# Optimization experiments

Hardware: AMD Instinct MI355X
Metric: run time of the kernel (lower is better)

The kernel has to match this reference:

```python
import jax, jax.numpy as jnp
import numpy as np

B, T, V, E, H, L = 128, 128, 5000, 256, 512, 128
PAD_IDX = 0


def setup_inputs() -> dict:
    key = jax.random.key(0)
    ks = jax.random.split(key, 12)
    s = 0.02  # init scale
    noise = jax.random.normal(ks[0], (B, L), dtype=jnp.float32)
    # Precomputed gumbel noise, one draw per (step, batch, vocab)
    u = jax.random.uniform(ks[1], (T, B, V), dtype=jnp.float32, minval=1e-9, maxval=1.0)
    gumbel = -jnp.log(-jnp.log(u))
    emb = (jax.random.normal(ks[2], (V, E), dtype=jnp.float32) * s).at[PAD_IDX].set(0.0)
    return {
        "noise": noise,
        "gumbel": gumbel,
        "temperature": jnp.float32(1.0),
        "W_init": jax.random.normal(ks[3], (H, L), dtype=jnp.float32) * s,
        "b_init": jnp.zeros((H,), dtype=jnp.float32),
        "emb": emb,
        "W_ih": jax.random.normal(ks[4], (3 * H, E), dtype=jnp.float32) * s,
        "W_hh": jax.random.normal(ks[5], (3 * H, H), dtype=jnp.float32) * s,
        "b_ih": jax.random.normal(ks[6], (3 * H,), dtype=jnp.float32) * s,
        "b_hh": jax.random.normal(ks[7], (3 * H,), dtype=jnp.float32) * s,
        "W_out": jax.random.normal(ks[8], (V, H), dtype=jnp.float32) * s,
        "b_out": jnp.zeros((V,), dtype=jnp.float32),
    }


def reference(noise, gumbel, temperature, W_init, b_init, emb, W_ih, W_hh, b_ih, b_hh, W_out, b_out):
    # h_0 = fc_initial_state(noise)  -> [B, H]
    h0 = noise @ W_init.T + b_init
    # first-step input: one-hot at pad_idx (embedding row PAD_IDX, which is zero)
    onehot0 = jnp.zeros((B, V), dtype=noise.dtype).at[:, PAD_IDX].set(1.0)
    tau = jnp.reshape(temperature, ())

    def step(carry, g):
        h, prev_onehot = carry
        x = prev_onehot @ emb                      # [B, E] soft-embedding feedback
        gi = x @ W_ih.T + b_ih                     # [B, 3H]
        gh = h @ W_hh.T + b_hh                     # [B, 3H]
        i_r, i_z, i_n = jnp.split(gi, 3, axis=-1)
        h_r, h_z, h_n = jnp.split(gh, 3, axis=-1)
        r = jax.nn.sigmoid(i_r + h_r)
        z = jax.nn.sigmoid(i_z + h_z)
        n = jnp.tanh(i_n + r * h_n)
        h_new = (1.0 - z) * n + z * h              # GRU cell (torch convention)
        # dropout is identity in eval mode
        logits = h_new @ W_out.T + b_out           # [B, V]
        y = jax.nn.softmax((logits + g) / tau, axis=-1)  # soft gumbel-softmax
        return (h_new, y), y

    _, ys = jax.lax.scan(step, (h0, onehot0), gumbel)  # ys: [T, B, V]
    return jnp.transpose(ys, (1, 0, 2))                # [B, T, V]
```

## Files before the change

kernel.cpp:

```cpp
#include <hip/hip_runtime.h>
#include <math.h>

#define Bq 128
#define Tq 128
#define Vq 5000
#define VP 5120
#define Eq 256
#define Hq 512
#define Lq 128
#define G3H 1536
#define KT 128
#define LROW 136

typedef __attribute__((ext_vector_type(8))) short bf16x8;
typedef __attribute__((ext_vector_type(4))) float f32x4;

__device__ __forceinline__ ushort f2bf(float f) {
    union { float f; unsigned u; } v; v.f = f;
    unsigned r = (v.u + 0x7FFFu + ((v.u >> 16) & 1u)) >> 16;
    return (ushort)r;
}
__device__ __forceinline__ float bf2f(ushort s) {
    union { unsigned u; float f; } v; v.u = ((unsigned)s) << 16;
    return v.f;
}
__device__ __forceinline__ float lof(unsigned u) {
    union { unsigned x; float f; } v; v.x = u << 16; return v.f;
}
__device__ __forceinline__ float hif(unsigned u) {
    union { unsigned x; float f; } v; v.x = u & 0xFFFF0000u; return v.f;
}
__device__ __forceinline__ float rcpf(float x) { return __builtin_amdgcn_rcpf(x); }

template<int MI>
__device__ __forceinline__ void macT(
    f32x4 (&acc)[MI][4],
    const ushort* __restrict__ A, int lda,
    const ushort* __restrict__ Bm, int ldb,
    int n0, int kbase, int Klen,
    ushort* As, ushort* Bs)
{
    const int NA = 2 * MI;
    const int tid = threadIdx.x;
    const int lane = tid & 63;
    const int w = tid >> 6;
    const int wm = (w >> 1) * (MI * 16);
    const int wn = (w & 1) * 64;
    const int fr = lane & 15;
    const int fk = (lane >> 4) * 8;

    int arow[NA], akc[NA];
    #pragma unroll
    for (int i = 0; i < NA; ++i) {
        int c = tid + i * 256;
        arow[i] = c >> 4; akc[i] = (c & 15) * 8;
    }
    int brow[8], bkc[8];
    #pragma unroll
    for (int i = 0; i < 8; ++i) {
        int c = tid + i * 256;
        brow[i] = c >> 4; bkc[i] = (c & 15) * 8;
    }

    const int nk = Klen / KT;
    bf16x8 ra[NA], rb[8];
    #pragma unroll
    for (int i = 0; i < NA; ++i)
        ra[i] = *(const bf16x8*)(A + (size_t)arow[i] * lda + kbase + akc[i]);
    #pragma unroll
    for (int i = 0; i < 8; ++i)
        rb[i] = *(const bf16x8*)(Bm + (size_t)(n0 + brow[i]) * ldb + kbase + bkc[i]);
    #pragma unroll
    for (int i = 0; i < NA; ++i)
        *(bf16x8*)(As + arow[i] * LROW + akc[i]) = ra[i];
    #pragma unroll
    for (int i = 0; i < 8; ++i)
        *(bf16x8*)(Bs + brow[i] * LROW + bkc[i]) = rb[i];
    __syncthreads();

    for (int kt = 0; kt < nk; ++kt) {
        if (kt + 1 < nk) {
            int kb = kbase + (kt + 1) * KT;
            #pragma unroll
            for (int i = 0; i < NA; ++i)
                ra[i] = *(const bf16x8*)(A + (size_t)arow[i] * lda + kb + akc[i]);
            #pragma unroll
            for (int i = 0; i < 8; ++i)
                rb[i] = *(const bf16x8*)(Bm + (size_t)(n0 + brow[i]) * ldb + kb + bkc[i]);
        }
        #pragma unroll
        for (int ks = 0; ks < 4; ++ks) {
            bf16x8 af[MI], bfv[4];
            const int ko = ks * 32 + fk;
            #pragma unroll
            for (int mi = 0; mi < MI; ++mi)
                af[mi] = *(const bf16x8*)(As + (wm + mi * 16 + fr) * LROW + ko);
            #pragma unroll
            for (int ni = 0; ni < 4; ++ni)
                bfv[ni] = *(const bf16x8*)(Bs + (wn + ni * 16 + fr) * LROW + ko);
            #pragma unroll
            for (int mi = 0; mi < MI; ++mi)
                #pragma unroll
                for (int ni = 0; ni < 4; ++ni)
                    acc[mi][ni] = __builtin_amdgcn_mfma_f32_16x16x32_bf16(
                        af[mi], bfv[ni], acc[mi][ni], 0, 0, 0);
        }
        __syncthreads();
        if (kt + 1 < nk) {
            #pragma unroll
            for (int i = 0; i < NA; ++i)
                *(bf16x8*)(As + arow[i] * LROW + akc[i]) = ra[i];
            #pragma unroll
            for (int i = 0; i < 8; ++i)
                *(bf16x8*)(Bs + brow[i] * LROW + bkc[i]) = rb[i];
            __syncthreads();
        }
    }
}

__device__ __forceinline__ void gh_block(
    int j, const ushort* __restrict__ hBsrc, const ushort* __restrict__ WhhB,
    ushort* __restrict__ ghp, ushort* As, ushort* Bs)
{
    const int tid = threadIdx.x;
    const int lane = tid & 63, w = tid >> 6;
    const int fr = lane & 15, hi = lane >> 4;
    const int nt = j >> 2, rem = j & 3;
    const int mh = rem >> 1, kc = rem & 1;
    const int n0 = nt * 128;
    const int wm = (w >> 1) * 32, wn = (w & 1) * 64;
    f32x4 acc[2][4];
    #pragma unroll
    for (int mi = 0; mi < 2; ++mi)
        #pragma unroll
        for (int ni = 0; ni < 4; ++ni) acc[mi][ni] = (f32x4){0.f,0.f,0.f,0.f};
    macT<2>(acc, hBsrc + (size_t)mh * 64 * Hq, Hq, WhhB, Hq,
            n0, kc * 256, 256, As, Bs);
    ushort* C = ghp + (size_t)kc * (Bq * G3H);
    #pragma unroll
    for (int mi = 0; mi < 2; ++mi)
        #pragma unroll
        for (int ni = 0; ni < 4; ++ni) {
            int n = n0 + wn + ni * 16 + fr;
            #pragma unroll
            for (int r = 0; r < 4; ++r) {
                int m = mh * 64 + wm + mi * 16 + hi * 4 + r;
                C[(size_t)m * G3H + n] = f2bf(acc[mi][ni][r]);
            }
        }
}

__device__ __forceinline__ void norm2s(
    int bpair, int tprev, float* __restrict__ out,
    const float* __restrict__ esl)
{
    const int tid = threadIdx.x;
    #pragma unroll
    for (int j = 0; j < 2; ++j) {
        int b = bpair * 2 + j;
        float S = 0.f;
        #pragma unroll 8
        for (int nt = 0; nt < 40; ++nt)
            S += esl[nt * 128 + b];
        float inv = 1.0f / S;
        float* orow = out + ((size_t)b * Tq + tprev) * Vq;
        #pragma unroll
        for (int i = 0; i < 20; ++i) {
            int v = tid + i * 256;
            if (v < Vq) orow[v] *= inv;
        }
    }
}

__global__ __launch_bounds__(256) void k_Q(
    const ushort* __restrict__ giP, const ushort* __restrict__ ghp,
    const float* __restrict__ b_ih, const float* __restrict__ b_hh,
    const float* __restrict__ h_old, const float* __restrict__ esumPrev,
    float* __restrict__ h_new, ushort* __restrict__ hB_new,
    float* __restrict__ out, int t)
{
    const int bid = blockIdx.x;
    const int tid = threadIdx.x;
    if (bid >= 128) {
        if (t > 0) norm2s(bid - 128, t - 1, out, esumPrev);
        return;
    }
    const int b = bid;
    float invS = 1.0f;
    if (t > 0) {
        float S = 0.f;
        #pragma unroll 8
        for (int q = 0; q < 40; ++q) S += esumPrev[q * 128 + b];
        invS = 1.0f / S;
    }
    const int i = tid * 2;
    const size_t o = (size_t)b * G3H + i;
    float xr0=0.f,xr1=0.f,xz0=0.f,xz1=0.f,xn0=0.f,xn1=0.f;
    #pragma unroll 8
    for (int z = 0; z < 40; ++z) {
        const ushort* gp = giP + (size_t)z * (Bq * G3H) + o;
        unsigned ur = *(const unsigned*)(gp);
        unsigned uz = *(const unsigned*)(gp + Hq);
        unsigned un = *(const unsigned*)(gp + 2 * Hq);
        xr0 += lof(ur); xr1 += hif(ur);
        xz0 += lof(uz); xz1 += hif(uz);
        xn0 += lof(un); xn1 += hif(un);
    }
    float2 bir = *(const float2*)(b_ih + i);
    float2 biz = *(const float2*)(b_ih + Hq + i);
    float2 bin = *(const float2*)(b_ih + 2 * Hq + i);
    xr0 = xr0 * invS + bir.x;  xr1 = xr1 * invS + bir.y;
    xz0 = xz0 * invS + biz.x;  xz1 = xz1 * invS + biz.y;
    xn0 = xn0 * invS + bin.x;  xn1 = xn1 * invS + bin.y;
    const ushort* h0p = ghp + o;
    const ushort* h1p = ghp + (size_t)(Bq * G3H) + o;
    unsigned a0r = *(const unsigned*)(h0p);
    unsigned a0z = *(const unsigned*)(h0p + Hq);
    unsigned a0n = *(const unsigned*)(h0p + 2 * Hq);
    unsigned a1r = *(const unsigned*)(h1p);
    unsigned a1z = *(const unsigned*)(h1p + Hq);
    unsigned a1n = *(const unsigned*)(h1p + 2 * Hq);
    float2 bhr = *(const float2*)(b_hh + i);
    float2 bhz = *(const float2*)(b_hh + Hq + i);
    float2 bhn = *(const float2*)(b_hh + 2 * Hq + i);
    float hr0 = bhr.x + lof(a0r) + lof(a1r);
    float hr1 = bhr.y + hif(a0r) + hif(a1r);
    float hz0 = bhz.x + lof(a0z) + lof(a1z);
    float hz1 = bhz.y + hif(a0z) + hif(a1z);
    float hn0 = bhn.x + lof(a0n) + lof(a1n);
    float hn1 = bhn.y + hif(a0n) + hif(a1n);
    float r0 = rcpf(1.f + __expf(-(xr0 + hr0)));
    float r1 = rcpf(1.f + __expf(-(xr1 + hr1)));
    float z0 = rcpf(1.f + __expf(-(xz0 + hz0)));
    float z1 = rcpf(1.f + __expf(-(xz1 + hz1)));
    float e0 = __expf(2.f * (xn0 + r0 * hn0));
    float e1 = __expf(2.f * (xn1 + r1 * hn1));
    float nn0 = 1.f - 2.f * rcpf(e0 + 1.f);
    float nn1 = 1.f - 2.f * rcpf(e1 + 1.f);
    float2 ho = *(const float2*)(h_old + (size_t)b * Hq + i);
    float hv0 = (1.f - z0) * nn0 + z0 * ho.x;
    float hv1 = (1.f - z1) * nn1 + z1 * ho.y;
    *(float2*)(h_new + (size_t)b * Hq + i) = make_float2(hv0, hv1);
    unsigned hb = (unsigned)f2bf(hv0) | ((unsigned)f2bf(hv1) << 16);
    *(unsigned*)(hB_new + (size_t)b * Hq + i) = hb;
}

__global__ __launch_bounds__(256) void k_P(
    const ushort* __restrict__ hBt, const ushort* __restrict__ WoutB,
    const ushort* __restrict__ WhhB, const ushort* __restrict__ WcombT,
    const float* __restrict__ b_out, const float* __restrict__ gum,
    const float* __restrict__ temp, float* __restrict__ out,
    float* __restrict__ esumCur, ushort* __restrict__ giP,
    ushort* __restrict__ ghp, int t)
{
    __shared__ __align__(16) ushort As[64 * LROW];
    __shared__ __align__(16) ushort Bs[128 * LROW];
    const int tid = threadIdx.x, bid = blockIdx.x;
    const int lane = tid & 63, w = tid >> 6;
    const int fr = lane & 15, hi = lane >> 4, fk = hi * 8;

    if (bid >= 160) {
        if (t + 1 < Tq)
            gh_block(bid - 160, hBt, WhhB, ghp, As, Bs);
        return;
    }
    const int nt = bid % 40, mq = bid / 40;
    const int b0 = mq * 32, ncol0 = nt * 128;
    const int wm = (w >> 1) * 16, wn = (w & 1) * 64;

    f32x4 acc[1][4];
    #pragma unroll
    for (int ni = 0; ni < 4; ++ni) acc[0][ni] = (f32x4){0.f,0.f,0.f,0.f};
    macT<1>(acc, hBt + (size_t)b0 * Hq, Hq, WoutB, Hq, ncol0, 0, Hq, As, Bs);

    const float inv_tau = 1.0f / temp[0];
    float psum[4] = {0.f, 0.f, 0.f, 0.f};
    #pragma unroll
    for (int ni = 0; ni < 4; ++ni) {
        int v = ncol0 + wn + ni * 16 + fr;
        bool valid = v < Vq;
        float bo = valid ? b_out[v] : 0.f;
        #pragma unroll
        for (int r = 0; r < 4; ++r) {
            int ml = wm + hi * 4 + r;
            int m = b0 + ml;
            float ev = 0.f;
            if (valid) {
                float g = gum[(size_t)m * Vq + v];
                ev = __expf((acc[0][ni][r] + bo + g) * inv_tau);
                out[(size_t)m * Tq * Vq + (size_t)t * Vq + v] = ev;
            }
            As[ml * LROW + (wn + ni * 16 + fr)] = f2bf(ev);
            psum[r] += ev;
        }
    }
    float* redbuf = (float*)Bs;
    #pragma unroll
    for (int r = 0; r < 4; ++r) {
        float s = psum[r];
        s += __shfl_xor(s, 1); s += __shfl_xor(s, 2);
        s += __shfl_xor(s, 4); s += __shfl_xor(s, 8);
        if (fr == 0)
            redbuf[((wm + hi * 4 + r) << 1) | (wn >> 6)] = s;
    }
    __syncthreads();
    if (tid < 32)
        esumCur[ncol0 + b0 + tid] = redbuf[tid * 2] + redbuf[tid * 2 + 1];

    if (t + 1 >= Tq) return;
    int brow[8], bkc[8];
    #pragma unroll
    for (int i = 0; i < 8; ++i) {
        int c = tid + i * 256;
        brow[i] = c >> 4; bkc[i] = (c & 15) * 8;
    }
    bf16x8 rb2[8];
    #pragma unroll
    for (int i = 0; i < 8; ++i)
        rb2[i] = *(const bf16x8*)(WcombT + (size_t)brow[i] * VP + ncol0 + bkc[i]);
    ushort* Pbase = giP + (size_t)nt * (Bq * G3H) + (size_t)b0 * G3H;
    for (int jt = 0; jt < 12; ++jt) {
        __syncthreads();
        #pragma unroll
        for (int i = 0; i < 8; ++i)
            *(bf16x8*)(Bs + brow[i] * LROW + bkc[i]) = rb2[i];
        __syncthreads();
        if (jt + 1 < 12) {
            #pragma unroll
            for (int i = 0; i < 8; ++i)
                rb2[i] = *(const bf16x8*)(WcombT +
                    (size_t)((jt + 1) * 128 + brow[i]) * VP + ncol0 + bkc[i]);
        }
        f32x4 pac[4];
        #pragma unroll
        for (int ni = 0; ni < 4; ++ni) pac[ni] = (f32x4){0.f,0.f,0.f,0.f};
        #pragma unroll
        for (int ks = 0; ks < 4; ++ks) {
            const int ko = ks * 32 + fk;
            bf16x8 af = *(const bf16x8*)(As + (wm + fr) * LROW + ko);
            #pragma unroll
            for (int ni = 0; ni < 4; ++ni) {
                bf16x8 bv = *(const bf16x8*)(Bs + (wn + ni * 16 + fr) * LROW + ko);
                pac[ni] = __builtin_amdgcn_mfma_f32_16x16x32_bf16(af, bv, pac[ni], 0, 0, 0);
            }
        }
        ushort* P = Pbase + jt * 128;
        #pragma unroll
        for (int ni = 0; ni < 4; ++ni) {
            int jl = wn + ni * 16 + fr;
            #pragma unroll
            for (int r = 0; r < 4; ++r) {
                int ml = wm + hi * 4 + r;
                P[(size_t)ml * G3H + jl] = f2bf(pac[ni][r]);
            }
        }
    }
}

__global__ __launch_bounds__(256) void k_prep(
    const float* __restrict__ W_ih, const float* __restrict__ W_hh,
    const float* __restrict__ W_out, const float* __restrict__ noise,
    const float* __restrict__ W_init, const float* __restrict__ emb,
    ushort* __restrict__ WihB, ushort* __restrict__ WhhB, ushort* __restrict__ WoutB,
    ushort* __restrict__ noiseB, ushort* __restrict__ WinitB,
    ushort* __restrict__ embB)
{
    const int tg = blockIdx.x * 256 + threadIdx.x;
    const int NTH = gridDim.x * 256;
    for (int i = tg; i < G3H * Eq / 4; i += NTH) {
        float4 f = *(const float4*)(W_ih + (size_t)i * 4);
        *(ushort4*)(WihB + (size_t)i * 4) =
            make_ushort4(f2bf(f.x), f2bf(f.y), f2bf(f.z), f2bf(f.w));
    }
    for (int i = tg; i < G3H * Hq / 4; i += NTH) {
        float4 f = *(const float4*)(W_hh + (size_t)i * 4);
        *(ushort4*)(WhhB + (size_t)i * 4) =
            make_ushort4(f2bf(f.x), f2bf(f.y), f2bf(f.z), f2bf(f.w));
    }
    for (int i = tg; i < VP * (Hq / 4); i += NTH) {
        int v = i >> 7, h4 = (i & 127) << 2;
        ushort4 o = make_ushort4(0, 0, 0, 0);
        if (v < Vq) {
            float4 f = *(const float4*)(W_out + (size_t)v * Hq + h4);
            o = make_ushort4(f2bf(f.x), f2bf(f.y), f2bf(f.z), f2bf(f.w));
        }
        *(ushort4*)(WoutB + (size_t)v * Hq + h4) = o;
    }
    for (int i = tg; i < VP * (Eq / 4); i += NTH) {
        int v = i >> 6, e4 = (i & 63) << 2;
        ushort4 o = make_ushort4(0, 0, 0, 0);
        if (v < Vq) {
            float4 f = *(const float4*)(emb + (size_t)v * Eq + e4);
            o = make_ushort4(f2bf(f.x), f2bf(f.y), f2bf(f.z), f2bf(f.w));
        }
        *(ushort4*)(embB + (size_t)v * Eq + e4) = o;
    }
    for (int i = tg; i < Bq * Lq / 4; i += NTH) {
        float4 f = *(const float4*)(noise + (size_t)i * 4);
        *(ushort4*)(noiseB + (size_t)i * 4) =
            make_ushort4(f2bf(f.x), f2bf(f.y), f2bf(f.z), f2bf(f.w));
    }
    for (int i = tg; i < Hq * Lq / 4; i += NTH) {
        float4 f = *(const float4*)(W_init + (size_t)i * 4);
        *(ushort4*)(WinitB + (size_t)i * 4) =
            make_ushort4(f2bf(f.x), f2bf(f.y), f2bf(f.z), f2bf(f.w));
    }
}

__global__ __launch_bounds__(256) void k_wh0(
    const ushort* __restrict__ WihB, const ushort* __restrict__ embB,
    const ushort* __restrict__ noiseB, const ushort* __restrict__ WinitB,
    const float* __restrict__ b_init,
    ushort* __restrict__ WcombT, float* __restrict__ h0, ushort* __restrict__ hB0)
{
    __shared__ __align__(16) ushort As[128 * LROW];
    __shared__ __align__(16) ushort Bs[128 * LROW];
    const int bid = blockIdx.x;
    const int lane = threadIdx.x & 63;
    const int w = threadIdx.x >> 6;
    const int wm = (w >> 1) * 64, wn = (w & 1) * 64;
    const int fr = lane & 15, hi = lane >> 4;
    f32x4 acc[4][4];
    #pragma unroll
    for (int mi = 0; mi < 4; ++mi)
        #pragma unroll
        for (int ni = 0; ni < 4; ++ni) acc[mi][ni] = (f32x4){0.f,0.f,0.f,0.f};
    if (bid < 480) {
        int mt = bid / 40, nt = bid % 40;
        macT<4>(acc, WihB + (size_t)mt * 128 * Eq, Eq, embB, Eq,
                nt * 128, 0, Eq, As, Bs);
        #pragma unroll
        for (int mi = 0; mi < 4; ++mi)
            #pragma unroll
            for (int ni = 0; ni < 4; ++ni) {
                int n = nt * 128 + wn + ni * 16 + fr;
                #pragma unroll
                for (int r = 0; r < 4; ++r) {
                    int m = mt * 128 + wm + mi * 16 + hi * 4 + r;
                    WcombT[(size_t)m * VP + n] = f2bf(acc[mi][ni][r]);
                }
            }
    } else {
        int n0 = (bid - 480) * 128;
        macT<4>(acc, noiseB, Lq, WinitB, Lq, n0, 0, Lq, As, Bs);
        #pragma unroll
        for (int mi = 0; mi < 4; ++mi)
            #pragma unroll
            for (int ni = 0; ni < 4; ++ni) {
                int n = n0 + wn + ni * 16 + fr;
                float bv = b_init[n];
                #pragma unroll
                for (int r = 0; r < 4; ++r) {
                    int m = wm + mi * 16 + hi * 4 + r;
                    float v = acc[mi][ni][r] + bv;
                    h0[(size_t)m * Hq + n] = v;
                    hB0[(size_t)m * Hq + n] = f2bf(v);
                }
            }
    }
}

__global__ __launch_bounds__(256) void k_gh0(
    const ushort* __restrict__ hB0, const ushort* __restrict__ WhhB,
    ushort* __restrict__ ghp, ushort* __restrict__ giP)
{
    __shared__ __align__(16) ushort As[64 * LROW];
    __shared__ __align__(16) ushort Bs[128 * LROW];
    const int bid = blockIdx.x;
    if (bid < 48) {
        gh_block(bid, hB0, WhhB, ghp, As, Bs);
    } else {
        const int zb = bid - 48;
        ushort4* p = (ushort4*)giP;
        const int total = 40 * Bq * G3H / 4;
        const int per = total / 192;
        int base = zb * per + threadIdx.x;
        #pragma unroll 8
        for (int k = 0; k < 40; ++k)
            p[base + k * 256] = make_ushort4(0, 0, 0, 0);
    }
}

__global__ __launch_bounds__(256) void k_tail(
    float* __restrict__ out, const float* __restrict__ esl)
{
    norm2s(blockIdx.x, Tq - 1, out, esl);
}

extern "C" void kernel_launch(void* const* d_in, const int* in_sizes, int n_in,
                              void* d_out, int out_size, void* d_ws, size_t ws_size,
                              hipStream_t stream)
{
    const float* noise   = (const float*)d_in[0];
    const float* gumbel  = (const float*)d_in[1];
    const float* temp    = (const float*)d_in[2];
    const float* W_init  = (const float*)d_in[3];
    const float* b_init  = (const float*)d_in[4];
    const float* emb     = (const float*)d_in[5];
    const float* W_ih    = (const float*)d_in[6];
    const float* W_hh    = (const float*)d_in[7];
    const float* b_ih    = (const float*)d_in[8];
    const float* b_hh    = (const float*)d_in[9];
    const float* W_out   = (const float*)d_in[10];
    const float* b_out   = (const float*)d_in[11];
    float* out = (float*)d_out;

    float* h       = (float*)d_ws;
    float* esum    = h + 131072;
    ushort* ub     = (ushort*)(esum + 10240);
    ushort* ghp    = ub;
    ushort* WhhB   = ghp + 393216;
    ushort* WoutB  = WhhB + 786432;
    ushort* WcombT = WoutB + 2621440;
    ushort* hB     = WcombT + 7864320;
    ushort* giP    = hB + 131072;
    ushort* embB   = giP;
    ushort* WihB   = embB + 1310720;
    ushort* noiseB = WihB + 393216;
    ushort* WinitB = noiseB + 16384;

    k_prep<<<dim3(512), dim3(256), 0, stream>>>(
        W_ih, W_hh, W_out, noise, W_init, emb,
        WihB, WhhB, WoutB, noiseB, WinitB, embB);
    k_wh0<<<dim3(484), dim3(256), 0, stream>>>(
        WihB, embB, noiseB, WinitB, b_init, WcombT, h, hB);
    k_gh0<<<dim3(240), dim3(256), 0, stream>>>(hB, WhhB, ghp, giP);

    for (int t = 0; t < Tq; ++t) {
        float* h_old = h + (size_t)(t & 1) * 65536;
        float* h_new = h + (size_t)((t + 1) & 1) * 65536;
        ushort* hB_new = hB + (size_t)((t + 1) & 1) * 65536;
        float* esumPrev = esum + (size_t)((t + 1) & 1) * 5120;
        float* esumCur  = esum + (size_t)(t & 1) * 5120;

        k_Q<<<dim3(192), dim3(256), 0, stream>>>(
            giP, ghp, b_ih, b_hh, h_old, esumPrev, h_new, hB_new, out, t);
        k_P<<<dim3(t + 1 < Tq ? 208 : 160), dim3(256), 0, stream>>>(
            hB_new, WoutB, WhhB, WcombT, b_out,
            gumbel + (size_t)t * Bq * Vq, temp,
            out, esumCur, giP, ghp, t);
    }
    k_tail<<<dim3(64), dim3(256), 0, stream>>>(
        out, esum + (size_t)((Tq - 1) & 1) * 5120);
}
```

Measured before the change: 4.104 ms.

## Double-buffer LDS tiles in k_P and stage P output through shared memory

Replaces the generic macT call in k_P with an inlined K loop that double-buffers A and B tiles in LDS, so the global loads for the next K slice overlap the MFMAs on the current one and one barrier per slice is saved. The giP projection loop is also double-buffered, dropping one of its two barriers per tile. Its bf16 results are staged in an LDS buffer and written as coalesced 16-byte stores one iteration later, instead of scattered 2-byte stores. LDS use per block roughly doubles, which may lower occupancy.

```diff
diff --git a/kernel.cpp b/kernel.cpp
--- a/kernel.cpp
+++ b/kernel.cpp
@@ -254,24 +254,80 @@
     ushort* __restrict__ ghp, int t)
 {
     __shared__ __align__(16) ushort As[64 * LROW];
-    __shared__ __align__(16) ushort Bs[128 * LROW];
+    __shared__ __align__(16) ushort Bs[2][128 * LROW];
+    __shared__ __align__(16) ushort Xs[2][32 * LROW];
     const int tid = threadIdx.x, bid = blockIdx.x;
     const int lane = tid & 63, w = tid >> 6;
     const int fr = lane & 15, hi = lane >> 4, fk = hi * 8;
 
     if (bid >= 160) {
         if (t + 1 < Tq)
-            gh_block(bid - 160, hBt, WhhB, ghp, As, Bs);
+            gh_block(bid - 160, hBt, WhhB, ghp, As, Bs[0]);
         return;
     }
     const int nt = bid % 40, mq = bid / 40;
     const int b0 = mq * 32, ncol0 = nt * 128;
     const int wm = (w >> 1) * 16, wn = (w & 1) * 64;
 
-    f32x4 acc[1][4];
-    #pragma unroll
-    for (int ni = 0; ni < 4; ++ni) acc[0][ni] = (f32x4){0.f,0.f,0.f,0.f};
-    macT<1>(acc, hBt + (size_t)b0 * Hq, Hq, WoutB, Hq, ncol0, 0, Hq, As, Bs);
+    int arow[2], akc[2], brow[8], bkc[8];
+    #pragma unroll
+    for (int i = 0; i < 2; ++i) { int c = tid + i * 256; arow[i] = c >> 4; akc[i] = (c & 15) * 8; }
+    #pragma unroll
+    for (int i = 0; i < 8; ++i) { int c = tid + i * 256; brow[i] = c >> 4; bkc[i] = (c & 15) * 8; }
+
+    const ushort* Abase = hBt + (size_t)b0 * Hq;
+    const ushort* Bbase = WoutB + (size_t)ncol0 * Hq;
+    bf16x8 ra[2], rb[8];
+    #pragma unroll
+    for (int i = 0; i < 2; ++i)
+        ra[i] = *(const bf16x8*)(Abase + (size_t)arow[i] * Hq + akc[i]);
+    #pragma unroll
+    for (int i = 0; i < 8; ++i)
+        rb[i] = *(const bf16x8*)(Bbase + (size_t)brow[i] * Hq + bkc[i]);
+    #pragma unroll
+    for (int i = 0; i < 2; ++i)
+        *(bf16x8*)(As + arow[i] * LROW + akc[i]) = ra[i];
+    #pragma unroll
+    for (int i = 0; i < 8; ++i)
+        *(bf16x8*)(Bs[0] + brow[i] * LROW + bkc[i]) = rb[i];
+    __syncthreads();
+
+    f32x4 acc[4];
+    #pragma unroll
+    for (int ni = 0; ni < 4; ++ni) acc[ni] = (f32x4){0.f,0.f,0.f,0.f};
+    int cur = 0;
+    for (int kt = 0; kt < 4; ++kt) {
+        if (kt < 3) {
+            const int kb = (kt + 1) * KT;
+            #pragma unroll
+            for (int i = 0; i < 2; ++i)
+                ra[i] = *(const bf16x8*)(Abase + (size_t)arow[i] * Hq + kb + akc[i]);
+            #pragma unroll
+            for (int i = 0; i < 8; ++i)
+                rb[i] = *(const bf16x8*)(Bbase + (size_t)brow[i] * Hq + kb + bkc[i]);
+        }
+        #pragma unroll
+        for (int ks = 0; ks < 4; ++ks) {
+            const int ko = ks * 32 + fk;
+            bf16x8 af = *(const bf16x8*)(As + (cur * 32 + wm + fr) * LROW + ko);
+            #pragma unroll
+            for (int ni = 0; ni < 4; ++ni) {
+                bf16x8 bfv = *(const bf16x8*)(Bs[cur] + (wn + ni * 16 + fr) * LROW + ko);
+                acc[ni] = __builtin_amdgcn_mfma_f32_16x16x32_bf16(af, bfv, acc[ni], 0, 0, 0);
+            }
+        }
+        if (kt < 3) {
+            const int alt = cur ^ 1;
+            #pragma unroll
+            for (int i = 0; i < 2; ++i)
+                *(bf16x8*)(As + (alt * 32 + arow[i]) * LROW + akc[i]) = ra[i];
+            #pragma unroll
+            for (int i = 0; i < 8; ++i)
+                *(bf16x8*)(Bs[alt] + brow[i] * LROW + bkc[i]) = rb[i];
+            __syncthreads();
+            cur = alt;
+        }
+    }
 
     const float inv_tau = 1.0f / temp[0];
     float psum[4] = {0.f, 0.f, 0.f, 0.f};
@@ -287,14 +343,14 @@
             float ev = 0.f;
             if (valid) {
                 float g = gum[(size_t)m * Vq + v];
-                ev = __expf((acc[0][ni][r] + bo + g) * inv_tau);
+                ev = __expf((acc[ni][r] + bo + g) * inv_tau);
                 out[(size_t)m * Tq * Vq + (size_t)t * Vq + v] = ev;
             }
             As[ml * LROW + (wn + ni * 16 + fr)] = f2bf(ev);
             psum[r] += ev;
         }
     }
-    float* redbuf = (float*)Bs;
+    float* redbuf = (float*)Xs[0];
     #pragma unroll
     for (int r = 0; r < 4; ++r) {
         float s = psum[r];
@@ -308,28 +364,33 @@
         esumCur[ncol0 + b0 + tid] = redbuf[tid * 2] + redbuf[tid * 2 + 1];
 
     if (t + 1 >= Tq) return;
-    int brow[8], bkc[8];
-    #pragma unroll
-    for (int i = 0; i < 8; ++i) {
-        int c = tid + i * 256;
-        brow[i] = c >> 4; bkc[i] = (c & 15) * 8;
-    }
-    bf16x8 rb2[8];
     #pragma unroll
     for (int i = 0; i < 8; ++i)
-        rb2[i] = *(const bf16x8*)(WcombT + (size_t)brow[i] * VP + ncol0 + bkc[i]);
+        rb[i] = *(const bf16x8*)(WcombT + (size_t)brow[i] * VP + ncol0 + bkc[i]);
+    #pragma unroll
+    for (int i = 0; i < 8; ++i)
+        *(bf16x8*)(Bs[0] + brow[i] * LROW + bkc[i]) = rb[i];
+    __syncthreads();
+
     ushort* Pbase = giP + (size_t)nt * (Bq * G3H) + (size_t)b0 * G3H;
+    int bcur = 0;
     for (int jt = 0; jt < 12; ++jt) {
-        __syncthreads();
-        #pragma unroll
-        for (int i = 0; i < 8; ++i)
-            *(bf16x8*)(Bs + brow[i] * LROW + bkc[i]) = rb2[i];
-        __syncthreads();
         if (jt + 1 < 12) {
             #pragma unroll
             for (int i = 0; i < 8; ++i)
-                rb2[i] = *(const bf16x8*)(WcombT +
+                rb[i] = *(const bf16x8*)(WcombT +
                     (size_t)((jt + 1) * 128 + brow[i]) * VP + ncol0 + bkc[i]);
+        }
+        if (jt > 0) {
+            const ushort* Xp = Xs[(jt - 1) & 1];
+            ushort* Pp = Pbase + (size_t)(jt - 1) * 128;
+            #pragma unroll
+            for (int q = 0; q < 2; ++q) {
+                int vv = tid + q * 256;
+                int r = vv >> 4, c8 = (vv & 15) * 8;
+                *(bf16x8*)(Pp + (size_t)r * G3H + c8) =
+                    *(const bf16x8*)(Xp + r * LROW + c8);
+            }
         }
         f32x4 pac[4];
         #pragma unroll
@@ -340,19 +401,34 @@
             bf16x8 af = *(const bf16x8*)(As + (wm + fr) * LROW + ko);
             #pragma unroll
             for (int ni = 0; ni < 4; ++ni) {
-                bf16x8 bv = *(const bf16x8*)(Bs + (wn + ni * 16 + fr) * LROW + ko);
+                bf16x8 bv = *(const bf16x8*)(Bs[bcur] + (wn + ni * 16 + fr) * LROW + ko);
                 pac[ni] = __builtin_amdgcn_mfma_f32_16x16x32_bf16(af, bv, pac[ni], 0, 0, 0);
             }
         }
-        ushort* P = Pbase + jt * 128;
+        ushort* Xc = Xs[jt & 1];
         #pragma unroll
         for (int ni = 0; ni < 4; ++ni) {
             int jl = wn + ni * 16 + fr;
             #pragma unroll
-            for (int r = 0; r < 4; ++r) {
-                int ml = wm + hi * 4 + r;
-                P[(size_t)ml * G3H + jl] = f2bf(pac[ni][r]);
-            }
+            for (int r = 0; r < 4; ++r)
+                Xc[(wm + hi * 4 + r) * LROW + jl] = f2bf(pac[ni][r]);
+        }
+        if (jt + 1 < 12) {
+            #pragma unroll
+            for (int i = 0; i < 8; ++i)
+                *(bf16x8*)(Bs[bcur ^ 1] + brow[i] * LROW + bkc[i]) = rb[i];
+        }
+        __syncthreads();
+        bcur ^= 1;
+    }
+    {
+        const ushort* Xp = Xs[1];
+        ushort* Pp = Pbase + (size_t)11 * 128;
+        #pragma unroll
+        for (int q = 0; q < 2; ++q) {
+            int vv = tid + q * 256;
+            int r = vv >> 4, c8 = (vv & 15) * 8;
+            *(bf16x8*)(Pp + (size_t)r * G3H + c8) = *(const bf16x8*)(Xp + r * LROW + c8);
         }
     }
 }
```

Measured after the change: 4.220 ms. 2.8% more time.
